# Kernel tuning notes

Hardware: AMD Instinct MI355X
Metric: run time of the kernel (lower is better)

## Reference

```python
import jax, jax.numpy as jnp
import numpy as np
from jax import lax

B, C, D, H, W = 2, 64, 16, 16, 16  # n = D*H*W = 4096; conv output length = n-2 = 4094
K = 3  # conv kernel size, dilation=2, padding=1


def setup_inputs() -> dict:
    key = jax.random.key(0)
    k1, k2, k3 = jax.random.split(key, 3)
    x = jax.random.normal(k1, (B, C, D, H, W), dtype=jnp.float32)
    # Conv1d params: weight [out_ch, in_ch, k], bias [out_ch]; PyTorch default init scale
    fan_in = C * K
    bound = 1.0 / np.sqrt(fan_in)
    conv_w = jax.random.uniform(k2, (C, C, K), jnp.float32, -bound, bound)
    conv_b = jax.random.uniform(k3, (C,), jnp.float32, -bound, bound)
    return {"x": x, "conv_w": conv_w, "conv_b": conv_b}


def _dspa(x, conv_w, conv_b):
    b, c, d, h, w = x.shape
    x1 = x.reshape(b, c, -1)  # [b, c, n]
    # dilated Conv1d: kernel=3, stride=1, padding=1, dilation=2 -> length n-2
    x2 = lax.conv_general_dilated(
        x1, conv_w,
        window_strides=(1,), padding=[(1, 1)], rhs_dilation=(2,),
        dimension_numbers=("NCH", "OIH", "NCH"),
    ) + conv_b[None, :, None]  # [b, c, n-2]
    # scores = bmm(x1^T, x2): [b, n, n-2]
    scores = jnp.einsum("bcn,bcm->bnm", x1, x2)
    # torch nn.Softmax() (dim=None) on a 3D tensor resolves to dim=0 (legacy behavior)
    x3 = jax.nn.softmax(scores, axis=0)  # [b, n, n-2]
    # x4 = bmm(x2, x3^T): [b, c, n]
    x4 = jnp.einsum("bcm,bnm->bcn", x2, x3)
    out = x1 + x4
    return out.reshape(b, c, d, h, w)


def reference(x, conv_w, conv_b):
    return _dspa(x, conv_w, conv_b)
```

## Files before the change

### kernel.cpp

```cpp
#include <hip/hip_runtime.h>

typedef unsigned short u16;
typedef unsigned int u32;
typedef __attribute__((ext_vector_type(8))) short bf16x8;
typedef __attribute__((ext_vector_type(4))) float f32x4;

#define NJ 4094

__device__ __forceinline__ u16 f2bf(float f) {
  union { float f; unsigned u; } v;
  v.f = f;
  unsigned r = v.u + 0x7fffu + ((v.u >> 16) & 1u);
  return (u16)(r >> 16);
}

__device__ __forceinline__ u32 pk_bf(float a, float b) {
  u32 ua = __float_as_uint(a) + 0x8000u;
  u32 ub = __float_as_uint(b) + 0x8000u;
  return __builtin_amdgcn_perm(ub, ua, 0x07060302u);
}

template <bool WRITE_OUT>
__global__ __launch_bounds__(256) void conv_kernel(
    const float* __restrict__ x, const float* __restrict__ w,
    const float* __restrict__ bias, u16* __restrict__ x2n, u16* __restrict__ x2T,
    float* __restrict__ out) {
  __shared__ float xs[64 * 36];
  __shared__ float wl[64 * 64 * 3];
  const int b = blockIdx.x >> 7, jt = blockIdx.x & 127;
  const int t = threadIdx.x;
  for (int idx = t; idx < 64 * 36; idx += 256) {
    int i = idx / 36, p = idx - i * 36;
    int jg = jt * 32 - 1 + p;
    float v = 0.f;
    if (jg >= 0 && jg < 4096) v = x[(b * 64 + i) * 4096 + jg];
    xs[idx] = v;
  }
  for (int idx = t; idx < 64 * 64 * 3; idx += 256) {
    int tap = idx % 3, ci = idx / 3;
    int c = ci >> 6, i = ci & 63;
    wl[(i * 64 + c) * 3 + tap] = w[idx];
  }
  __syncthreads();
  if (WRITE_OUT) {
    for (int idx = t; idx < 64 * 32; idx += 256) {
      int i = idx >> 5, k = idx & 31;
      out[(b * 64 + i) * 4096 + jt * 32 + k] = xs[i * 36 + k + 1];
    }
  }
  const int c = t & 63, jsub = t >> 6;
  float acc[8];
  float bv = bias[c];
#pragma unroll
  for (int k = 0; k < 8; k++) acc[k] = bv;
  for (int i = 0; i < 64; i++) {
    float w0 = wl[(i * 64 + c) * 3 + 0];
    float w1 = wl[(i * 64 + c) * 3 + 1];
    float w2 = wl[(i * 64 + c) * 3 + 2];
    const float* xr = &xs[i * 36 + jsub * 8];
#pragma unroll
    for (int k = 0; k < 8; k++)
      acc[k] += w0 * xr[k] + w1 * xr[k + 2] + w2 * xr[k + 4];
  }
#pragma unroll
  for (int k = 0; k < 8; k++) {
    int jg = jt * 32 + jsub * 8 + k;
    float v = (jg < NJ) ? acc[k] : 0.f;
    u16 hv = f2bf(v);
    x2n[(b * 64 + c) * 4096 + jg] = hv;
    x2T[(b * 4096 + jg) * 64 + c] = hv;
  }
}

template <bool ATOMIC>
__global__ __launch_bounds__(256, 4) void fused_kernel(
    const float* __restrict__ x, const u16* __restrict__ x2n_g,
    const u16* __restrict__ x2T_g, float* __restrict__ part_g,
    float* __restrict__ out) {
  __shared__ u16 P[2][2 * 64 * 72];
  const int t = threadIdx.x;
  const int wave = t >> 6, lane = t & 63;
  const int q = lane >> 4, ln = lane & 15;
  const int i0 = blockIdx.x * 64;
  const int jc = blockIdx.y;

  u16* xs = P[1];
#pragma unroll
  for (int rep = 0; rep < 32; rep++) {
    int idx = rep * 256 + t;
    int il = idx & 63, c = (idx >> 6) & 63, b = idx >> 12;
    float v = x[(b * 64 + c) * 4096 + i0 + il];
    if (b) v = -v;
    xs[(b * 64 + il) * 72 + c] = f2bf(v);
  }
  __syncthreads();

  bf16x8 b1[2][4][2];
#pragma unroll
  for (int b = 0; b < 2; b++)
#pragma unroll
    for (int ist = 0; ist < 4; ist++)
#pragma unroll
      for (int kc = 0; kc < 2; kc++)
        b1[b][ist][kc] = *(const bf16x8*)&xs[(b * 64 + ist * 16 + ln) * 72 + kc * 32 + q * 8];

  f32x4 acc[2][4];
#pragma unroll
  for (int a = 0; a < 2; a++)
#pragma unroll
    for (int bq = 0; bq < 4; bq++) acc[a][bq] = (f32x4){0.f, 0.f, 0.f, 0.f};

  const int b2 = wave >> 1, cs2 = (wave & 1) * 2;

  for (int jt = jc * 4; jt < jc * 4 + 4; jt++) {
    const int j0 = jt * 64;
    u16* Ps = P[jt & 1];
    f32x4 ps[4];
#pragma unroll
    for (int ist = 0; ist < 4; ist++) ps[ist] = (f32x4){0.f, 0.f, 0.f, 0.f};
#pragma unroll
    for (int b = 0; b < 2; b++)
#pragma unroll
      for (int kc = 0; kc < 2; kc++) {
        bf16x8 af = *(const bf16x8*)&x2T_g[(b * 4096 + j0 + wave * 16 + ln) * 64 + kc * 32 + q * 8];
#pragma unroll
        for (int ist = 0; ist < 4; ist++)
          ps[ist] = __builtin_amdgcn_mfma_f32_16x16x32_bf16(af, b1[b][ist][kc], ps[ist], 0, 0, 0);
      }
#pragma unroll
    for (int ist = 0; ist < 4; ist++) {
      float p0[4], p1[4];
#pragma unroll
      for (int r = 0; r < 4; r++) {
        float e = __expf(-ps[ist][r]);
        p0[r] = __builtin_amdgcn_rcpf(1.f + e);
        p1[r] = 1.f - p0[r];
      }
      uint2 o0 = make_uint2(pk_bf(p0[0], p0[1]), pk_bf(p0[2], p0[3]));
      uint2 o1 = make_uint2(pk_bf(p1[0], p1[1]), pk_bf(p1[2], p1[3]));
      *(uint2*)&Ps[(0 + ist * 16 + ln) * 72 + wave * 16 + q * 4] = o0;
      *(uint2*)&Ps[(64 + ist * 16 + ln) * 72 + wave * 16 + q * 4] = o1;
    }
    __syncthreads();
#pragma unroll
    for (int kc = 0; kc < 2; kc++) {
      bf16x8 af2[2], pb[4];
#pragma unroll
      for (int cst = 0; cst < 2; cst++)
        af2[cst] = *(const bf16x8*)&x2n_g[(b2 * 64 + (cs2 + cst) * 16 + ln) * 4096 + j0 + kc * 32 + q * 8];
#pragma unroll
      for (int ist = 0; ist < 4; ist++)
        pb[ist] = *(const bf16x8*)&Ps[(b2 * 64 + ist * 16 + ln) * 72 + kc * 32 + q * 8];
#pragma unroll
      for (int cst = 0; cst < 2; cst++)
#pragma unroll
        for (int ist = 0; ist < 4; ist++)
          acc[cst][ist] =
              __builtin_amdgcn_mfma_f32_16x16x32_bf16(af2[cst], pb[ist], acc[cst][ist], 0, 0, 0);
    }
  }
#pragma unroll
  for (int cst = 0; cst < 2; cst++)
#pragma unroll
    for (int ist = 0; ist < 4; ist++)
#pragma unroll
      for (int r = 0; r < 4; r++) {
        int c = (cs2 + cst) * 16 + q * 4 + r;
        int ii = i0 + ist * 16 + ln;
        if (ATOMIC) {
          unsafeAtomicAdd(&out[(b2 * 64 + c) * 4096 + ii], acc[cst][ist][r]);
        } else {
          part_g[(((jc * 2 + b2) * 64 + c) << 12) + ii] = acc[cst][ist][r];
        }
      }
}

__global__ __launch_bounds__(256) void reduce_kernel(
    const float4* __restrict__ x, const float4* __restrict__ part,
    float4* __restrict__ out) {
  int i = blockIdx.x * 256 + threadIdx.x;
  float4 s = x[i];
#pragma unroll
  for (int jc = 0; jc < 16; jc++) {
    float4 p = part[jc * 131072 + i];
    s.x += p.x; s.y += p.y; s.z += p.z; s.w += p.w;
  }
  out[i] = s;
}

extern "C" void kernel_launch(void* const* d_in, const int* in_sizes, int n_in,
                              void* d_out, int out_size, void* d_ws, size_t ws_size,
                              hipStream_t stream) {
  const float* x = (const float*)d_in[0];
  const float* w = (const float*)d_in[1];
  const float* bias = (const float*)d_in[2];
  float* out = (float*)d_out;
  u16* x2n = (u16*)d_ws;
  u16* x2T = x2n + 2 * 64 * 4096;
  float* part = (float*)(x2T + 2 * 64 * 4096);

  const size_t need = 2u * 64 * 4096 * 2 * 2 + 16u * 2 * 64 * 4096 * 4;
  dim3 grid(64, 16);
  if (ws_size >= need) {
    conv_kernel<false><<<256, 256, 0, stream>>>(x, w, bias, x2n, x2T, out);
    fused_kernel<false><<<grid, 256, 0, stream>>>(x, x2n, x2T, part, out);
    reduce_kernel<<<512, 256, 0, stream>>>((const float4*)x, (const float4*)part, (float4*)out);
  } else {
    conv_kernel<true><<<256, 256, 0, stream>>>(x, w, bias, x2n, x2T, out);
    fused_kernel<true><<<grid, 256, 0, stream>>>(x, x2n, x2T, nullptr, out);
  }
}
```

Baseline: 107.5 us.

## Split conv into smaller tiles, pad weight LDS, and prefetch x2n in fused kernel

The conv kernel now handles 16 output positions per block instead of 32, launching 512 blocks with 4 outputs per thread. The weight table in LDS uses a padded [i][c*3+tap] layout with stride 195 to avoid bank conflicts, and x2n is stored with a vectorized ushort4 write. In the fused kernel, the first x2n fragment for the second GEMM is loaded before the softmax/LDS-store phase to hide global load latency. The cost is more redundant weight loading into LDS across twice as many conv blocks.

```diff
diff --git a/kernel.cpp b/kernel.cpp
--- a/kernel.cpp
+++ b/kernel.cpp
@@ -20,56 +20,60 @@
   return __builtin_amdgcn_perm(ub, ua, 0x07060302u);
 }
 
+#define WST 195
 template <bool WRITE_OUT>
 __global__ __launch_bounds__(256) void conv_kernel(
     const float* __restrict__ x, const float* __restrict__ w,
     const float* __restrict__ bias, u16* __restrict__ x2n, u16* __restrict__ x2T,
     float* __restrict__ out) {
-  __shared__ float xs[64 * 36];
-  __shared__ float wl[64 * 64 * 3];
-  const int b = blockIdx.x >> 7, jt = blockIdx.x & 127;
+  __shared__ float xs[64 * 20];
+  __shared__ float wl[64 * WST];
+  const int b = blockIdx.x >> 8, jt = blockIdx.x & 255;
   const int t = threadIdx.x;
-  for (int idx = t; idx < 64 * 36; idx += 256) {
-    int i = idx / 36, p = idx - i * 36;
-    int jg = jt * 32 - 1 + p;
+  for (int idx = t; idx < 64 * 20; idx += 256) {
+    int i = idx / 20, p = idx - i * 20;
+    int jg = jt * 16 - 1 + p;
     float v = 0.f;
     if (jg >= 0 && jg < 4096) v = x[(b * 64 + i) * 4096 + jg];
     xs[idx] = v;
   }
   for (int idx = t; idx < 64 * 64 * 3; idx += 256) {
-    int tap = idx % 3, ci = idx / 3;
-    int c = ci >> 6, i = ci & 63;
-    wl[(i * 64 + c) * 3 + tap] = w[idx];
+    int c = idx / 192, r = idx - c * 192;
+    int i = r / 3, tap = r - i * 3;
+    wl[i * WST + c * 3 + tap] = w[idx];
   }
   __syncthreads();
   if (WRITE_OUT) {
-    for (int idx = t; idx < 64 * 32; idx += 256) {
-      int i = idx >> 5, k = idx & 31;
-      out[(b * 64 + i) * 4096 + jt * 32 + k] = xs[i * 36 + k + 1];
+    for (int idx = t; idx < 64 * 16; idx += 256) {
+      int i = idx >> 4, k = idx & 15;
+      out[(b * 64 + i) * 4096 + jt * 16 + k] = xs[i * 20 + k + 1];
     }
   }
   const int c = t & 63, jsub = t >> 6;
-  float acc[8];
   float bv = bias[c];
-#pragma unroll
-  for (int k = 0; k < 8; k++) acc[k] = bv;
+  float a0 = bv, a1 = bv, a2 = bv, a3 = bv;
   for (int i = 0; i < 64; i++) {
-    float w0 = wl[(i * 64 + c) * 3 + 0];
-    float w1 = wl[(i * 64 + c) * 3 + 1];
-    float w2 = wl[(i * 64 + c) * 3 + 2];
-    const float* xr = &xs[i * 36 + jsub * 8];
-#pragma unroll
-    for (int k = 0; k < 8; k++)
-      acc[k] += w0 * xr[k] + w1 * xr[k + 2] + w2 * xr[k + 4];
-  }
-#pragma unroll
-  for (int k = 0; k < 8; k++) {
-    int jg = jt * 32 + jsub * 8 + k;
-    float v = (jg < NJ) ? acc[k] : 0.f;
-    u16 hv = f2bf(v);
-    x2n[(b * 64 + c) * 4096 + jg] = hv;
-    x2T[(b * 4096 + jg) * 64 + c] = hv;
-  }
+    const float* wr = &wl[i * WST + c * 3];
+    float w0 = wr[0], w1 = wr[1], w2 = wr[2];
+    const float* xr = &xs[i * 20 + jsub * 4];
+    float x0 = xr[0], x1 = xr[1], x2 = xr[2], x3 = xr[3];
+    float x4 = xr[4], x5 = xr[5], x6 = xr[6], x7 = xr[7];
+    a0 += w0 * x0 + w1 * x2 + w2 * x4;
+    a1 += w0 * x1 + w1 * x3 + w2 * x5;
+    a2 += w0 * x2 + w1 * x4 + w2 * x6;
+    a3 += w0 * x3 + w1 * x5 + w2 * x7;
+  }
+  const int jg0 = jt * 16 + jsub * 4;
+  float av[4] = {a0, a1, a2, a3};
+  ushort4 hv;
+  u16* hp = (u16*)&hv;
+#pragma unroll
+  for (int k = 0; k < 4; k++) {
+    float v = (jg0 + k < NJ) ? av[k] : 0.f;
+    hp[k] = f2bf(v);
+    x2T[(b * 4096 + jg0 + k) * 64 + c] = hp[k];
+  }
+  *(ushort4*)&x2n[(b * 64 + c) * 4096 + jg0] = hv;
 }
 
 template <bool ATOMIC>
@@ -127,6 +131,10 @@
         for (int ist = 0; ist < 4; ist++)
           ps[ist] = __builtin_amdgcn_mfma_f32_16x16x32_bf16(af, b1[b][ist][kc], ps[ist], 0, 0, 0);
       }
+    bf16x8 af2k0[2];
+#pragma unroll
+    for (int cst = 0; cst < 2; cst++)
+      af2k0[cst] = *(const bf16x8*)&x2n_g[(b2 * 64 + (cs2 + cst) * 16 + ln) * 4096 + j0 + q * 8];
 #pragma unroll
     for (int ist = 0; ist < 4; ist++) {
       float p0[4], p1[4];
@@ -147,7 +155,9 @@
       bf16x8 af2[2], pb[4];
 #pragma unroll
       for (int cst = 0; cst < 2; cst++)
-        af2[cst] = *(const bf16x8*)&x2n_g[(b2 * 64 + (cs2 + cst) * 16 + ln) * 4096 + j0 + kc * 32 + q * 8];
+        af2[cst] = (kc == 0)
+                       ? af2k0[cst]
+                       : *(const bf16x8*)&x2n_g[(b2 * 64 + (cs2 + cst) * 16 + ln) * 4096 + j0 + kc * 32 + q * 8];
 #pragma unroll
       for (int ist = 0; ist < 4; ist++)
         pb[ist] = *(const bf16x8*)&Ps[(b2 * 64 + ist * 16 + ln) * 72 + kc * 32 + q * 8];
@@ -202,11 +212,11 @@
   const size_t need = 2u * 64 * 4096 * 2 * 2 + 16u * 2 * 64 * 4096 * 4;
   dim3 grid(64, 16);
   if (ws_size >= need) {
-    conv_kernel<false><<<256, 256, 0, stream>>>(x, w, bias, x2n, x2T, out);
+    conv_kernel<false><<<512, 256, 0, stream>>>(x, w, bias, x2n, x2T, out);
     fused_kernel<false><<<grid, 256, 0, stream>>>(x, x2n, x2T, part, out);
     reduce_kernel<<<512, 256, 0, stream>>>((const float4*)x, (const float4*)part, (float4*)out);
   } else {
-    conv_kernel<true><<<256, 256, 0, stream>>>(x, w, bias, x2n, x2T, out);
+    conv_kernel<true><<<512, 256, 0, stream>>>(x, w, bias, x2n, x2T, out);
     fused_kernel<true><<<grid, 256, 0, stream>>>(x, x2n, x2T, nullptr, out);
   }
 }
```

Result: faster. 105.4 us (-2.0%).
